# Kernel optimization log

Measured on AMD Instinct MI355X. Metric: run time of the kernel, lower is better.

The kernel has to match this reference:

```python
import jax, jax.numpy as jnp
import numpy as np
from jax import lax

EPSILON = 0.1   # entropic regularization (init arg)
MAX_ITER = 100  # numItermax (init arg); stopThr ignored -> fixed iterations (jit-friendly)


def setup_inputs() -> dict:
    key = jax.random.key(0)
    k1, k2 = jax.random.split(key)
    n, m, d = 8192, 8192, 64
    x = jax.random.uniform(k1, (n, d), dtype=jnp.float32)
    y = jax.random.uniform(k2, (m, d), dtype=jnp.float32)
    return {"x": x, "y": y}


def _cdist(x, y):
    # euclidean distance matrix, torch.cdist(p=2)
    sq = (jnp.sum(x * x, axis=1)[:, None]
          + jnp.sum(y * y, axis=1)[None, :]
          - 2.0 * (x @ y.T))
    return jnp.sqrt(jnp.clip(sq, 1e-12))


def reference(x, y):
    n, m = x.shape[0], y.shape[0]
    C = _cdist(x, y)                       # [n, m]
    K = jnp.exp(-C / EPSILON)              # Gibbs kernel [n, m]
    a = jnp.full((n,), 1.0 / n, dtype=x.dtype)  # uniform marginals (POT default)
    b = jnp.full((m,), 1.0 / m, dtype=y.dtype)
    u0 = jnp.full((n,), 1.0 / n, dtype=x.dtype)

    def body(i, u):
        v = b / (K.T @ u)
        return a / (K @ v)

    u = lax.fori_loop(0, MAX_ITER, body, u0)
    v = b / (K.T @ u)
    pi = u[:, None] * K * v[None, :]       # transport plan [n, m]
    return pi
```

## Files before the change

### kernel.cpp

```cpp
#include <hip/hip_runtime.h>
#include <hip/hip_bf16.h>

#define NN 8192
#define DD 64
#define NITER 100

typedef unsigned short u16;
typedef unsigned int u32;

static constexpr float INV_EPS = 10.0f;
static constexpr float MARG    = 1.0f / 8192.0f;

__device__ __forceinline__ void unpack8(const uint4 q, float f[8]) {
  f[0] = __uint_as_float(q.x << 16); f[1] = __uint_as_float(q.x & 0xffff0000u);
  f[2] = __uint_as_float(q.y << 16); f[3] = __uint_as_float(q.y & 0xffff0000u);
  f[4] = __uint_as_float(q.z << 16); f[5] = __uint_as_float(q.z & 0xffff0000u);
  f[6] = __uint_as_float(q.w << 16); f[7] = __uint_as_float(q.w & 0xffff0000u);
}

__global__ __launch_bounds__(256) void norms_k(const float* __restrict__ x,
                                               const float* __restrict__ y,
                                               float* __restrict__ xx,
                                               float* __restrict__ yy) {
  int idx = blockIdx.x * 256 + threadIdx.x;
  const float* src = (idx < NN) ? (x + (size_t)idx * DD)
                                : (y + (size_t)(idx - NN) * DD);
  const float4* p = (const float4*)src;
  float s = 0.f;
#pragma unroll
  for (int i = 0; i < 16; i++) {
    float4 v = p[i];
    s += v.x * v.x + v.y * v.y + v.z * v.z + v.w * v.w;
  }
  if (idx < NN) xx[idx] = s; else yy[idx - NN] = s;
}

__global__ __launch_bounds__(256) void build_k(const float* __restrict__ x,
                                               const float* __restrict__ y,
                                               const float* __restrict__ xx,
                                               const float* __restrict__ yy,
                                               u16* __restrict__ K) {
  __shared__ float xs[64][64];
  __shared__ float ys[64][128];

  int t  = threadIdx.x;
  int ib = blockIdx.x & 127;
  int jb = blockIdx.x >> 7;
  int i0 = ib * 64;
  int j0 = jb * 128;

  {
    int row = t >> 2, kc = (t & 3) * 16;
    const float4* src = (const float4*)(x + (size_t)(i0 + row) * DD + kc);
#pragma unroll
    for (int c = 0; c < 4; c++) {
      float4 v = src[c];
      xs[kc + c * 4 + 0][row] = v.x;
      xs[kc + c * 4 + 1][row] = v.y;
      xs[kc + c * 4 + 2][row] = v.z;
      xs[kc + c * 4 + 3][row] = v.w;
    }
  }
  {
    int col = t >> 1, kc = (t & 1) * 32;
    const float4* src = (const float4*)(y + (size_t)(j0 + col) * DD + kc);
#pragma unroll
    for (int c = 0; c < 8; c++) {
      float4 v = src[c];
      ys[kc + c * 4 + 0][col] = v.x;
      ys[kc + c * 4 + 1][col] = v.y;
      ys[kc + c * 4 + 2][col] = v.z;
      ys[kc + c * 4 + 3][col] = v.w;
    }
  }
  __syncthreads();

  int tr = (t >> 4) * 4;
  int tc = (t & 15) * 8;

  float acc[4][8];
#pragma unroll
  for (int r = 0; r < 4; r++)
#pragma unroll
    for (int c = 0; c < 8; c++) acc[r][c] = 0.f;

#pragma unroll 4
  for (int k = 0; k < DD; k++) {
    float4 xa = *(const float4*)&xs[k][tr];
    float4 y0 = *(const float4*)&ys[k][tc];
    float4 y1 = *(const float4*)&ys[k][tc + 4];
    float xv[4] = {xa.x, xa.y, xa.z, xa.w};
    float yv[8] = {y0.x, y0.y, y0.z, y0.w, y1.x, y1.y, y1.z, y1.w};
#pragma unroll
    for (int r = 0; r < 4; r++)
#pragma unroll
      for (int c = 0; c < 8; c++) acc[r][c] += xv[r] * yv[c];
  }

  float xn[4], yn[8];
#pragma unroll
  for (int r = 0; r < 4; r++) xn[r] = xx[i0 + tr + r];
#pragma unroll
  for (int c = 0; c < 8; c++) yn[c] = yy[j0 + tc + c];

#pragma unroll
  for (int r = 0; r < 4; r++) {
    u16 outp[8];
#pragma unroll
    for (int c = 0; c < 8; c++) {
      float sq = xn[r] + yn[c] - 2.f * acc[r][c];
      sq = fmaxf(sq, 1e-12f);
      float kv = __expf(-sqrtf(sq) * INV_EPS);
      __hip_bfloat16 h = __float2bfloat16(kv);
      outp[c] = *reinterpret_cast<u16*>(&h);
    }
    *(uint4*)(K + (size_t)(i0 + tr + r) * NN + j0 + tc) = *(uint4*)outp;
  }
}

__global__ __launch_bounds__(256) void col0_k(const u16* __restrict__ K,
                                              float* __restrict__ P) {
  int t = threadIdx.x;
  int b = blockIdx.x;
  int i0 = b * 16;
  float acc[4][8];
#pragma unroll
  for (int c = 0; c < 4; c++)
#pragma unroll
    for (int e = 0; e < 8; e++) acc[c][e] = 0.f;

  for (int r = 0; r < 16; r++) {
#pragma unroll
    for (int c = 0; c < 4; c++) {
      uint4 q = *(const uint4*)(K + (size_t)(i0 + r) * NN + c * 2048 + t * 8);
      float f[8];
      unpack8(q, f);
#pragma unroll
      for (int e = 0; e < 8; e++) acc[c][e] += f[e];
    }
  }
#pragma unroll
  for (int c = 0; c < 4; c++) {
    float4 lo = {acc[c][0] * MARG, acc[c][1] * MARG, acc[c][2] * MARG, acc[c][3] * MARG};
    float4 hi = {acc[c][4] * MARG, acc[c][5] * MARG, acc[c][6] * MARG, acc[c][7] * MARG};
    float* dst = P + (size_t)b * NN + c * 2048 + t * 8;
    *(float4*)dst = lo;
    *(float4*)(dst + 4) = hi;
  }
}

__global__ __launch_bounds__(256) void red_k(const float* __restrict__ P,
                                             float* __restrict__ v) {
  int t = threadIdx.x;
  int j0 = blockIdx.x * 32;
  int jj = t & 31;
  int kk = t >> 5;
  float s = 0.f;
#pragma unroll 8
  for (int k = kk * 64; k < kk * 64 + 64; k++)
    s += P[(size_t)k * NN + j0 + jj];
  __shared__ float red[256];
  red[t] = s;
  __syncthreads();
  if (t < 32) {
    float tot = 0.f;
#pragma unroll
    for (int k = 0; k < 8; k++) tot += red[k * 32 + t];
    v[j0 + t] = MARG / tot;
  }
}

__global__ __launch_bounds__(256) void fused_k(const u16* __restrict__ K,
                                               const float* __restrict__ vin,
                                               float* __restrict__ uout,
                                               float* __restrict__ P) {
  int t = threadIdx.x;
  int b = blockIdx.x;
  int i0 = b * 16;

  float vv[4][8];
#pragma unroll
  for (int c = 0; c < 4; c++) {
    const float* vp = vin + c * 2048 + t * 8;
    float4 a = *(const float4*)vp;
    float4 bq = *(const float4*)(vp + 4);
    vv[c][0] = a.x;  vv[c][1] = a.y;  vv[c][2] = a.z;  vv[c][3] = a.w;
    vv[c][4] = bq.x; vv[c][5] = bq.y; vv[c][6] = bq.z; vv[c][7] = bq.w;
  }

  float acc[4][8];
#pragma unroll
  for (int c = 0; c < 4; c++)
#pragma unroll
    for (int e = 0; e < 8; e++) acc[c][e] = 0.f;

  __shared__ float red[2][256];
  __shared__ float ubc[2];

  for (int rb = 0; rb < 8; rb++) {
    int i = i0 + rb * 2;
    uint4 q0[4], q1[4];
#pragma unroll
    for (int c = 0; c < 4; c++) {
      q0[c] = *(const uint4*)(K + (size_t)i * NN + c * 2048 + t * 8);
      q1[c] = *(const uint4*)(K + (size_t)(i + 1) * NN + c * 2048 + t * 8);
    }
    float s0 = 0.f, s1 = 0.f;
#pragma unroll
    for (int c = 0; c < 4; c++) {
      float f[8];
      unpack8(q0[c], f);
#pragma unroll
      for (int e = 0; e < 8; e++) s0 += f[e] * vv[c][e];
      unpack8(q1[c], f);
#pragma unroll
      for (int e = 0; e < 8; e++) s1 += f[e] * vv[c][e];
    }
    red[0][t] = s0;
    red[1][t] = s1;
    __syncthreads();
    int w = t >> 6, l = t & 63;
    if (w < 2) {
      float val = red[w][l] + red[w][l + 64] + red[w][l + 128] + red[w][l + 192];
#pragma unroll
      for (int o = 32; o > 0; o >>= 1) val += __shfl_xor(val, o);
      if (l == 0) {
        float uv = MARG / val;
        uout[i + w] = uv;
        ubc[w] = uv;
      }
    }
    __syncthreads();
    float u0 = ubc[0], u1 = ubc[1];
#pragma unroll
    for (int c = 0; c < 4; c++) {
      float f[8];
      unpack8(q0[c], f);
#pragma unroll
      for (int e = 0; e < 8; e++) acc[c][e] += f[e] * u0;
      unpack8(q1[c], f);
#pragma unroll
      for (int e = 0; e < 8; e++) acc[c][e] += f[e] * u1;
    }
  }

#pragma unroll
  for (int c = 0; c < 4; c++) {
    float4 lo = {acc[c][0], acc[c][1], acc[c][2], acc[c][3]};
    float4 hi = {acc[c][4], acc[c][5], acc[c][6], acc[c][7]};
    float* dst = P + (size_t)b * NN + c * 2048 + t * 8;
    *(float4*)dst = lo;
    *(float4*)(dst + 4) = hi;
  }
}

__global__ __launch_bounds__(256) void pi_k(const u16* __restrict__ K,
                                            const float* __restrict__ u,
                                            const float* __restrict__ v,
                                            float* __restrict__ out) {
  int t = threadIdx.x;
  int b = blockIdx.x;
  int i0 = b * 16;

  float vv[4][8];
#pragma unroll
  for (int c = 0; c < 4; c++) {
    const float* vp = v + c * 2048 + t * 8;
    float4 a = *(const float4*)vp;
    float4 bq = *(const float4*)(vp + 4);
    vv[c][0] = a.x;  vv[c][1] = a.y;  vv[c][2] = a.z;  vv[c][3] = a.w;
    vv[c][4] = bq.x; vv[c][5] = bq.y; vv[c][6] = bq.z; vv[c][7] = bq.w;
  }

  for (int r = 0; r < 16; r++) {
    int i = i0 + r;
    float uv = u[i];
#pragma unroll
    for (int c = 0; c < 4; c++) {
      uint4 q = *(const uint4*)(K + (size_t)i * NN + c * 2048 + t * 8);
      float f[8];
      unpack8(q, f);
      float4 lo = {uv * f[0] * vv[c][0], uv * f[1] * vv[c][1],
                   uv * f[2] * vv[c][2], uv * f[3] * vv[c][3]};
      float4 hi = {uv * f[4] * vv[c][4], uv * f[5] * vv[c][5],
                   uv * f[6] * vv[c][6], uv * f[7] * vv[c][7]};
      float* dst = out + (size_t)i * NN + c * 2048 + t * 8;
      *(float4*)dst = lo;
      *(float4*)(dst + 4) = hi;
    }
  }
}

extern "C" void kernel_launch(void* const* d_in, const int* in_sizes, int n_in,
                              void* d_out, int out_size, void* d_ws, size_t ws_size,
                              hipStream_t stream) {
  const float* x = (const float*)d_in[0];
  const float* y = (const float*)d_in[1];
  float* out = (float*)d_out;

  char* ws = (char*)d_ws;
  u16*  K  = (u16*)ws;
  float* P = (float*)(ws + (size_t)NN * NN * 2);
  float* xx = (float*)(ws + (size_t)NN * NN * 2 + (size_t)512 * NN * 4);
  float* yy = xx + NN;
  float* u  = yy + NN;
  float* v  = u + NN;

  norms_k<<<(2 * NN) / 256, 256, 0, stream>>>(x, y, xx, yy);
  build_k<<<128 * 64, 256, 0, stream>>>(x, y, xx, yy, K);
  col0_k<<<NN / 16, 256, 0, stream>>>(K, P);

  for (int it = 0; it < NITER; it++) {
    red_k<<<NN / 32, 256, 0, stream>>>(P, v);
    fused_k<<<NN / 16, 256, 0, stream>>>(K, v, u, P);
  }
  red_k<<<NN / 32, 256, 0, stream>>>(P, v);
  pi_k<<<NN / 16, 256, 0, stream>>>(K, u, v, out);
}
```

Before: 3.708 ms.

## Store partial column sums in bf16, prefetch K rows, batch row reductions

The per-block partial column-sum buffer P is now written and read as bf16 instead of fp32, which halves the traffic of that intermediate in every iteration. The fused kernel now handles 4 rows per group with wave-level shuffle reductions and a single barrier per group, and it prefetches the next 4 rows of K into registers so loads overlap compute. The final pi kernel launches more blocks with fewer rows each. The bf16 partial sums lose precision in the v update, and the larger register footprint may lower occupancy.

```diff
diff --git a/kernel.cpp b/kernel.cpp
--- a/kernel.cpp
+++ b/kernel.cpp
@@ -16,6 +16,11 @@
   f[2] = __uint_as_float(q.y << 16); f[3] = __uint_as_float(q.y & 0xffff0000u);
   f[4] = __uint_as_float(q.z << 16); f[5] = __uint_as_float(q.z & 0xffff0000u);
   f[6] = __uint_as_float(q.w << 16); f[7] = __uint_as_float(q.w & 0xffff0000u);
+}
+
+__device__ __forceinline__ u32 pkbf2(float a, float b) {
+  __hip_bfloat16 ha = __float2bfloat16(a), hb = __float2bfloat16(b);
+  return (u32)*reinterpret_cast<u16*>(&ha) | ((u32)*reinterpret_cast<u16*>(&hb) << 16);
 }
 
 __global__ __launch_bounds__(256) void norms_k(const float* __restrict__ x,
@@ -119,7 +124,7 @@
 }
 
 __global__ __launch_bounds__(256) void col0_k(const u16* __restrict__ K,
-                                              float* __restrict__ P) {
+                                              u16* __restrict__ P) {
   int t = threadIdx.x;
   int b = blockIdx.x;
   int i0 = b * 16;
@@ -141,42 +146,52 @@
   }
 #pragma unroll
   for (int c = 0; c < 4; c++) {
-    float4 lo = {acc[c][0] * MARG, acc[c][1] * MARG, acc[c][2] * MARG, acc[c][3] * MARG};
-    float4 hi = {acc[c][4] * MARG, acc[c][5] * MARG, acc[c][6] * MARG, acc[c][7] * MARG};
-    float* dst = P + (size_t)b * NN + c * 2048 + t * 8;
-    *(float4*)dst = lo;
-    *(float4*)(dst + 4) = hi;
-  }
-}
-
-__global__ __launch_bounds__(256) void red_k(const float* __restrict__ P,
+    uint4 w;
+    w.x = pkbf2(acc[c][0] * MARG, acc[c][1] * MARG);
+    w.y = pkbf2(acc[c][2] * MARG, acc[c][3] * MARG);
+    w.z = pkbf2(acc[c][4] * MARG, acc[c][5] * MARG);
+    w.w = pkbf2(acc[c][6] * MARG, acc[c][7] * MARG);
+    *(uint4*)(P + (size_t)b * NN + c * 2048 + t * 8) = w;
+  }
+}
+
+__global__ __launch_bounds__(256) void red_k(const u16* __restrict__ P,
                                              float* __restrict__ v) {
   int t = threadIdx.x;
   int j0 = blockIdx.x * 32;
-  int jj = t & 31;
-  int kk = t >> 5;
-  float s = 0.f;
+  int jjp = t & 15;
+  int kk  = t >> 4;
+  float s0 = 0.f, s1 = 0.f;
 #pragma unroll 8
-  for (int k = kk * 64; k < kk * 64 + 64; k++)
-    s += P[(size_t)k * NN + j0 + jj];
-  __shared__ float red[256];
-  red[t] = s;
+  for (int k = kk * 32; k < kk * 32 + 32; k++) {
+    u32 w = *(const u32*)(P + (size_t)k * NN + j0 + jjp * 2);
+    s0 += __uint_as_float(w << 16);
+    s1 += __uint_as_float(w & 0xffff0000u);
+  }
+  __shared__ float red[256][2];
+  red[t][0] = s0;
+  red[t][1] = s1;
   __syncthreads();
-  if (t < 32) {
-    float tot = 0.f;
-#pragma unroll
-    for (int k = 0; k < 8; k++) tot += red[k * 32 + t];
-    v[j0 + t] = MARG / tot;
-  }
-}
-
-__global__ __launch_bounds__(256) void fused_k(const u16* __restrict__ K,
-                                               const float* __restrict__ vin,
-                                               float* __restrict__ uout,
-                                               float* __restrict__ P) {
+  if (t < 16) {
+    float t0 = 0.f, t1 = 0.f;
+#pragma unroll
+    for (int k = 0; k < 16; k++) {
+      t0 += red[k * 16 + t][0];
+      t1 += red[k * 16 + t][1];
+    }
+    v[j0 + t * 2]     = MARG / t0;
+    v[j0 + t * 2 + 1] = MARG / t1;
+  }
+}
+
+__global__ __launch_bounds__(256, 2) void fused_k(const u16* __restrict__ K,
+                                                  const float* __restrict__ vin,
+                                                  float* __restrict__ uout,
+                                                  u16* __restrict__ P) {
   int t = threadIdx.x;
   int b = blockIdx.x;
   int i0 = b * 16;
+  int wave = t >> 6;
 
   float vv[4][8];
 #pragma unroll
@@ -194,63 +209,88 @@
 #pragma unroll
     for (int e = 0; e < 8; e++) acc[c][e] = 0.f;
 
-  __shared__ float red[2][256];
-  __shared__ float ubc[2];
-
-  for (int rb = 0; rb < 8; rb++) {
-    int i = i0 + rb * 2;
-    uint4 q0[4], q1[4];
-#pragma unroll
-    for (int c = 0; c < 4; c++) {
-      q0[c] = *(const uint4*)(K + (size_t)i * NN + c * 2048 + t * 8);
-      q1[c] = *(const uint4*)(K + (size_t)(i + 1) * NN + c * 2048 + t * 8);
-    }
-    float s0 = 0.f, s1 = 0.f;
-#pragma unroll
-    for (int c = 0; c < 4; c++) {
-      float f[8];
-      unpack8(q0[c], f);
-#pragma unroll
-      for (int e = 0; e < 8; e++) s0 += f[e] * vv[c][e];
-      unpack8(q1[c], f);
-#pragma unroll
-      for (int e = 0; e < 8; e++) s1 += f[e] * vv[c][e];
-    }
-    red[0][t] = s0;
-    red[1][t] = s1;
+  __shared__ float wsum[2][4][4];
+
+  uint4 q[4][4];
+#pragma unroll
+  for (int r = 0; r < 4; r++)
+#pragma unroll
+    for (int c = 0; c < 4; c++)
+      q[r][c] = *(const uint4*)(K + (size_t)(i0 + r) * NN + c * 2048 + t * 8);
+
+#pragma unroll
+  for (int rg = 0; rg < 4; rg++) {
+    int ibase = i0 + rg * 4;
+    uint4 qn[4][4];
+    if (rg < 3) {
+#pragma unroll
+      for (int r = 0; r < 4; r++)
+#pragma unroll
+        for (int c = 0; c < 4; c++)
+          qn[r][c] = *(const uint4*)(K + (size_t)(ibase + 4 + r) * NN + c * 2048 + t * 8);
+    }
+
+    float s[4];
+#pragma unroll
+    for (int r = 0; r < 4; r++) {
+      float sr = 0.f;
+#pragma unroll
+      for (int c = 0; c < 4; c++) {
+        float f[8];
+        unpack8(q[r][c], f);
+#pragma unroll
+        for (int e = 0; e < 8; e++) sr += f[e] * vv[c][e];
+      }
+      s[r] = sr;
+    }
+#pragma unroll
+    for (int r = 0; r < 4; r++) {
+#pragma unroll
+      for (int o = 32; o > 0; o >>= 1) s[r] += __shfl_xor(s[r], o);
+    }
+    if ((t & 63) == 0) {
+#pragma unroll
+      for (int r = 0; r < 4; r++) wsum[rg & 1][wave][r] = s[r];
+    }
     __syncthreads();
-    int w = t >> 6, l = t & 63;
-    if (w < 2) {
-      float val = red[w][l] + red[w][l + 64] + red[w][l + 128] + red[w][l + 192];
-#pragma unroll
-      for (int o = 32; o > 0; o >>= 1) val += __shfl_xor(val, o);
-      if (l == 0) {
-        float uv = MARG / val;
-        uout[i + w] = uv;
-        ubc[w] = uv;
+
+    float uu[4];
+#pragma unroll
+    for (int r = 0; r < 4; r++) {
+      float tot = wsum[rg & 1][0][r] + wsum[rg & 1][1][r]
+                + wsum[rg & 1][2][r] + wsum[rg & 1][3][r];
+      uu[r] = MARG / tot;
+    }
+    if (t < 4) uout[ibase + t] = uu[t];
+
+#pragma unroll
+    for (int r = 0; r < 4; r++) {
+#pragma unroll
+      for (int c = 0; c < 4; c++) {
+        float f[8];
+        unpack8(q[r][c], f);
+#pragma unroll
+        for (int e = 0; e < 8; e++) acc[c][e] += f[e] * uu[r];
       }
     }
-    __syncthreads();
-    float u0 = ubc[0], u1 = ubc[1];
-#pragma unroll
-    for (int c = 0; c < 4; c++) {
-      float f[8];
-      unpack8(q0[c], f);
-#pragma unroll
-      for (int e = 0; e < 8; e++) acc[c][e] += f[e] * u0;
-      unpack8(q1[c], f);
-#pragma unroll
-      for (int e = 0; e < 8; e++) acc[c][e] += f[e] * u1;
+
+    if (rg < 3) {
+#pragma unroll
+      for (int r = 0; r < 4; r++)
+#pragma unroll
+        for (int c = 0; c < 4; c++)
+          q[r][c] = qn[r][c];
     }
   }
 
 #pragma unroll
   for (int c = 0; c < 4; c++) {
-    float4 lo = {acc[c][0], acc[c][1], acc[c][2], acc[c][3]};
-    float4 hi = {acc[c][4], acc[c][5], acc[c][6], acc[c][7]};
-    float* dst = P + (size_t)b * NN + c * 2048 + t * 8;
-    *(float4*)dst = lo;
-    *(float4*)(dst + 4) = hi;
+    uint4 w;
+    w.x = pkbf2(acc[c][0], acc[c][1]);
+    w.y = pkbf2(acc[c][2], acc[c][3]);
+    w.z = pkbf2(acc[c][4], acc[c][5]);
+    w.w = pkbf2(acc[c][6], acc[c][7]);
+    *(uint4*)(P + (size_t)b * NN + c * 2048 + t * 8) = w;
   }
 }
 
@@ -260,7 +300,7 @@
                                             float* __restrict__ out) {
   int t = threadIdx.x;
   int b = blockIdx.x;
-  int i0 = b * 16;
+  int i0 = b * 4;
 
   float vv[4][8];
 #pragma unroll
@@ -272,7 +312,8 @@
     vv[c][4] = bq.x; vv[c][5] = bq.y; vv[c][6] = bq.z; vv[c][7] = bq.w;
   }
 
-  for (int r = 0; r < 16; r++) {
+#pragma unroll
+  for (int r = 0; r < 4; r++) {
     int i = i0 + r;
     float uv = u[i];
 #pragma unroll
@@ -300,8 +341,8 @@
 
   char* ws = (char*)d_ws;
   u16*  K  = (u16*)ws;
-  float* P = (float*)(ws + (size_t)NN * NN * 2);
-  float* xx = (float*)(ws + (size_t)NN * NN * 2 + (size_t)512 * NN * 4);
+  u16*  P  = (u16*)(ws + (size_t)NN * NN * 2);
+  float* xx = (float*)(ws + (size_t)NN * NN * 2 + (size_t)512 * NN * 2);
   float* yy = xx + NN;
   float* u  = yy + NN;
   float* v  = u + NN;
@@ -315,5 +356,5 @@
     fused_k<<<NN / 16, 256, 0, stream>>>(K, v, u, P);
   }
   red_k<<<NN / 32, 256, 0, stream>>>(P, v);
-  pi_k<<<NN / 16, 256, 0, stream>>>(K, u, v, out);
-}
+  pi_k<<<NN / 4, 256, 0, stream>>>(K, u, v, out);
+}
```

Measured after the change: 13.40 ms. +261.4%, slower.
